# Kernel optimization log

Hardware: AMD Instinct MI355X
Metric: run time of the kernel (lower is better)

Reference implementation:

```python
import jax, jax.numpy as jnp
import numpy as np

B, S, E, H, D = 2, 2048, 768, 12, 64  # batch, seq, emb_dim, num_heads, encoder_emb_dim
EPS = 1e-5


def setup_inputs() -> dict:
    key = jax.random.key(0)
    ks = jax.random.split(key, 6)
    # kaiming-uniform-ish bound for fan_in=E
    bound = float(np.sqrt(6.0 / E))
    u = lambda k, shp: jax.random.uniform(k, shp, jnp.float32, -bound, bound)
    return {
        "x": jax.random.normal(ks[0], (B, S, E), jnp.float32),
        "ln_w": jnp.ones((E,), jnp.float32),
        "ln_b": jnp.zeros((E,), jnp.float32),
        "wq": u(ks[1], (E, H * D)),
        "bq": jnp.zeros((H * D,), jnp.float32),
        "wk": u(ks[2], (E, H * D)),
        "bk": jnp.zeros((H * D,), jnp.float32),
        "wv": u(ks[3], (E, H * D)),
        "bv": jnp.zeros((H * D,), jnp.float32),
        "wo": u(ks[4], (H * D, E)),
        "bo": jnp.zeros((E,), jnp.float32),
    }


def reference(x, ln_w, ln_b, wq, bq, wk, bk, wv, bv, wo, bo):
    b, s, _ = x.shape
    # LayerNorm (biased variance, eps=1e-5), as torch.nn.LayerNorm
    mu = x.mean(-1, keepdims=True)
    var = ((x - mu) ** 2).mean(-1, keepdims=True)
    xn = (x - mu) * jax.lax.rsqrt(var + EPS) * ln_w + ln_b

    q = (xn @ wq + bq).reshape(b, s, H, D)
    k = (xn @ wk + bk).reshape(b, s, H, D)
    v = (xn @ wv + bv).reshape(b, s, H, D)

    scale = 1.0 / np.sqrt(D).astype(np.float32)
    scores = jnp.einsum("bihd,bjhd->bhij", q, k) * scale  # [B,H,S,S]

    # masking=True, self_attending=True: mask STRICTLY lower triangle with -inf
    # (i.e. each position attends only to itself and FUTURE positions)
    mask = jnp.tril(jnp.ones((s, s), dtype=bool), k=-1)
    scores = jnp.where(mask, -jnp.inf, scores)

    a = jax.nn.softmax(scores, axis=-1)
    h = jnp.einsum("bhij,bjhd->bihd", a, v).reshape(b, s, H * D)
    return h @ wo + bo
```

## Files before the change

kernel.cpp:

```cpp
#include <hip/hip_runtime.h>

typedef __bf16 bf16_t;
typedef __bf16 bf16x8 __attribute__((ext_vector_type(8)));
typedef __bf16 bf16x4 __attribute__((ext_vector_type(4)));
typedef short  s16x4  __attribute__((ext_vector_type(4)));
typedef float  f32x4  __attribute__((ext_vector_type(4)));
typedef unsigned int u32;

#define BB 2
#define SS 2048
#define EE 768
#define HH 12
#define DD 64
#define NROW (BB*SS)

#define GLDS16(gp, lp) __builtin_amdgcn_global_load_lds( \
    (const __attribute__((address_space(1))) u32*)(gp),   \
    (__attribute__((address_space(3))) u32*)(lp), 16, 0, 0)

#if __has_builtin(__builtin_amdgcn_mfma_f32_16x16x16bf16_1k)
#define MFMA16_BUILTIN 1
static __device__ __forceinline__ f32x4 mfma_16x16x16_bf16(bf16x4 a, bf16x4 b, f32x4 c) {
  return __builtin_amdgcn_mfma_f32_16x16x16bf16_1k(
      __builtin_bit_cast(s16x4, a), __builtin_bit_cast(s16x4, b), c, 0, 0, 0);
}
#else
#define MFMA16_BUILTIN 0
static __device__ __forceinline__ f32x4 mfma_16x16x16_bf16(bf16x4 a, bf16x4 b, f32x4 c) {
  asm volatile("v_mfma_f32_16x16x16_bf16 %0, %1, %2, %0" : "+v"(c) : "v"(a), "v"(b));
  return c;
}
#endif

__global__ __launch_bounds__(256) void pack_w_kernel(
    const float* __restrict__ wq, const float* __restrict__ wk,
    const float* __restrict__ wv, const float* __restrict__ wo,
    bf16_t* __restrict__ wt)
{
  __shared__ float tile[64][65];
  const float* src = (blockIdx.z==0)?wq:(blockIdx.z==1)?wk:(blockIdx.z==2)?wv:wo;
  const int k0 = blockIdx.x*64, n0 = blockIdx.y*64;
  const int t = threadIdx.x;
  #pragma unroll
  for (int it=0; it<16; ++it) {
    int idx = it*256+t, r = idx>>6, c = idx&63;
    tile[r][c] = src[(size_t)(k0+r)*EE + n0 + c];
  }
  __syncthreads();
  bf16_t* dst = wt + (size_t)blockIdx.z*EE*EE;
  #pragma unroll
  for (int it=0; it<16; ++it) {
    int idx = it*256+t, r = idx>>6, c = idx&63;
    dst[(size_t)(n0+r)*EE + k0 + c] = (bf16_t)tile[c][r];
  }
}

__global__ __launch_bounds__(256) void ln_kernel(
    const float* __restrict__ x, const float* __restrict__ w,
    const float* __restrict__ bvec, bf16_t* __restrict__ xn)
{
  const int row = blockIdx.x, t = threadIdx.x;
  const float* xr = x + (size_t)row*EE;
  float v0 = xr[t], v1 = xr[t+256], v2 = xr[t+512];
  float s  = v0+v1+v2;
  float ss = v0*v0 + v1*v1 + v2*v2;
  #pragma unroll
  for (int m=1; m<64; m<<=1) { s += __shfl_xor(s,m); ss += __shfl_xor(ss,m); }
  __shared__ float red[2][4];
  const int wid = t>>6, lane = t&63;
  if (lane==0) { red[0][wid]=s; red[1][wid]=ss; }
  __syncthreads();
  s  = red[0][0]+red[0][1]+red[0][2]+red[0][3];
  ss = red[1][0]+red[1][1]+red[1][2]+red[1][3];
  const float mu   = s*(1.0f/EE);
  const float rstd = rsqrtf(ss*(1.0f/EE) - mu*mu + 1e-5f);
  bf16_t* xo = xn + (size_t)row*EE;
  xo[t      ] = (bf16_t)((v0-mu)*rstd*w[t      ] + bvec[t      ]);
  xo[t + 256] = (bf16_t)((v1-mu)*rstd*w[t + 256] + bvec[t + 256]);
  xo[t + 512] = (bf16_t)((v2-mu)*rstd*w[t + 512] + bvec[t + 512]);
}

__global__ __launch_bounds__(256) void gemm_qkv_kernel(
    const bf16_t* __restrict__ xn, const bf16_t* __restrict__ wt,
    const float* __restrict__ bq, const float* __restrict__ bk, const float* __restrict__ bv,
    bf16_t* __restrict__ qb, bf16_t* __restrict__ kb, bf16_t* __restrict__ vb)
{
  __shared__ __align__(16) bf16_t As[2][128][32];
  __shared__ __align__(16) bf16_t Bs[2][128][32];
  const int bm = blockIdx.x, by = blockIdx.y;
  const int mat = by/6, nb = by%6;
  const bf16_t* W = wt + (size_t)mat*EE*EE + (size_t)nb*128*EE;
  const float* bias = (mat==0)?bq:(mat==1)?bk:bv;
  bf16_t* outp = (mat==0)?qb:(mat==1)?kb:vb;
  const int t = threadIdx.x, lane = t&63, wid = t>>6;
  const int wr = wid>>1, wc = wid&1;
  const int lrow = lane&15, lk = lane>>4;
  const bf16_t* Ag = xn + (size_t)bm*128*EE;

  const int srow = t>>2, sp = t&3;
  const int sg = sp ^ ((srow>>1)&3);
  const int pcs = (lrow>>1)&3;

  auto stage = [&](int buf, int k0) {
    const bf16_t* asrc = Ag + (size_t)srow*EE + k0 + sg*8;
    const bf16_t* bsrc = W  + (size_t)srow*EE + k0 + sg*8;
    GLDS16(asrc,                 &As[buf][0][0] + t*8);
    GLDS16(asrc + (size_t)64*EE, &As[buf][0][0] + 2048 + t*8);
    GLDS16(bsrc,                 &Bs[buf][0][0] + t*8);
    GLDS16(bsrc + (size_t)64*EE, &Bs[buf][0][0] + 2048 + t*8);
  };

  f32x4 acc[4][4];
  #pragma unroll
  for (int i=0;i<4;++i)
    #pragma unroll
    for (int j=0;j<4;++j) acc[i][j] = (f32x4){0.f,0.f,0.f,0.f};

  stage(0, 0);
  __syncthreads();
  int cur = 0;
  for (int k0=0; k0<EE; k0+=32) {
    if (k0+32 < EE) stage(cur^1, k0+32);
    bf16x8 af[4], bfv[4];
    #pragma unroll
    for (int mi=0;mi<4;++mi) af[mi]  = *(const bf16x8*)&As[cur][wr*64+mi*16+lrow][(lk^pcs)*8];
    #pragma unroll
    for (int ni=0;ni<4;++ni) bfv[ni] = *(const bf16x8*)&Bs[cur][wc*64+ni*16+lrow][(lk^pcs)*8];
    #pragma unroll
    for (int mi=0;mi<4;++mi)
      #pragma unroll
      for (int ni=0;ni<4;++ni)
        acc[mi][ni] = __builtin_amdgcn_mfma_f32_16x16x32_bf16(af[mi], bfv[ni], acc[mi][ni], 0,0,0);
    __syncthreads();
    cur ^= 1;
  }
  const int m_base = bm*128 + wr*64;
  const int n_base = nb*128 + wc*64;
  #pragma unroll
  for (int ni=0;ni<4;++ni) {
    const int col = n_base + ni*16 + lrow;
    const float bias_v = bias[col];
    #pragma unroll
    for (int mi=0;mi<4;++mi) {
      #pragma unroll
      for (int r=0;r<4;++r) {
        int row = m_base + mi*16 + 4*lk + r;
        outp[(size_t)row*EE + col] = (bf16_t)(acc[mi][ni][r] + bias_v);
      }
    }
  }
}

__global__ __launch_bounds__(256) void vtrans_kernel(
    const bf16_t* __restrict__ v, bf16_t* __restrict__ vt)
{
  __shared__ __align__(16) bf16_t tile[64][72];
  const int j0 = blockIdx.x*64, bh = blockIdx.y;
  const int b = bh/HH, h = bh%HH;
  const int t = threadIdx.x;
  #pragma unroll
  for (int it=0; it<2; ++it) {
    int idx = it*256+t, r = idx>>3, c8 = (idx&7)*8;
    *(bf16x8*)&tile[r][c8] = *(const bf16x8*)(v + (size_t)(b*SS + j0 + r)*EE + h*DD + c8);
  }
  __syncthreads();
  #pragma unroll
  for (int it=0; it<2; ++it) {
    int idx = it*256+t, d = idx>>3, c8 = (idx&7)*8;
    bf16x8 val;
    #pragma unroll
    for (int i=0;i<8;++i) val[i] = tile[c8+i][d];
    *(bf16x8*)(vt + ((size_t)bh*DD + d)*SS + j0 + c8) = val;
  }
}

__global__ __launch_bounds__(256) void attn_kernel(
    const bf16_t* __restrict__ qb, const bf16_t* __restrict__ kb,
    const bf16_t* __restrict__ vt, bf16_t* __restrict__ hb)
{
  __shared__ __align__(16) bf16_t Ks[2][64][64];
  __shared__ __align__(16) bf16_t Vts[2][64][64];

  const int bid = blockIdx.x;
  const int rnd = bid >> 8, g = bid & 255;
  const int item = (rnd == 1) ? (511 - g) : (rnd*256 + g);
  const int qt = item / 24, bh = item % 24;

  const int i0 = qt*64, b = bh/HH, h = bh%HH;
  const int t = threadIdx.x, lane = t&63, wid = t>>6;
  const int lrow = lane&15, lk = lane>>4;

  const int srow = t>>3, sp = t&7;
  const int sgc = sp ^ (srow&7);
  const bf16_t* kbase  = kb + (size_t)b*SS*EE + h*DD;
  const bf16_t* vtbase = vt + (size_t)bh*DD*SS;

  const bf16_t* qrow = qb + (size_t)(b*SS + i0 + wid*16 + lrow)*EE + h*DD;
  const bf16x8 qf0 = *(const bf16x8*)(qrow + lk*8);
  const bf16x8 qf1 = *(const bf16x8*)(qrow + 32 + lk*8);

  f32x4 acc_ot[4];
  #pragma unroll
  for (int i=0;i<4;++i) acc_ot[i] = (f32x4){0.f,0.f,0.f,0.f};
  float lsum = 0.f;
  const int iloc = wid*16 + lrow;
  const int kkey = lrow&7;

  auto stage = [&](int buf, int jt) {
    const int j0v = jt*64;
    const bf16_t* ksrc = kbase  + (size_t)(j0v + srow)*EE + sgc*8;
    const bf16_t* vsrc = vtbase + (size_t)srow*SS + j0v + sgc*8;
    GLDS16(ksrc,                 &Ks[buf][0][0]  + t*8);
    GLDS16(ksrc + (size_t)32*EE, &Ks[buf][0][0]  + 2048 + t*8);
    GLDS16(vsrc,                 &Vts[buf][0][0] + t*8);
    GLDS16(vsrc + (size_t)32*SS, &Vts[buf][0][0] + 2048 + t*8);
  };

#define ATTN_TILE(CUR, MASKED) do {                                          \
    float e[4][4];                                                           \
    _Pragma("unroll")                                                        \
    for (int sj=0;sj<4;++sj) {                                               \
      const bf16_t* krow = &Ks[CUR][sj*16+lrow][0];                          \
      bf16x8 kf0 = *(const bf16x8*)(krow + ((lk^kkey)<<3));                  \
      bf16x8 kf1 = *(const bf16x8*)(krow + (((lk+4)^kkey)<<3));              \
      f32x4 a = (f32x4){0.f,0.f,0.f,0.f};                                    \
      a = __builtin_amdgcn_mfma_f32_16x16x32_bf16(kf0, qf0, a, 0,0,0);       \
      a = __builtin_amdgcn_mfma_f32_16x16x32_bf16(kf1, qf1, a, 0,0,0);       \
      _Pragma("unroll")                                                      \
      for (int r=0;r<4;++r) {                                                \
        float ee = a[r]*0.180336878f - 34.6246784f;                          \
        if (MASKED && (sj*16 + 4*lk + r) < iloc) ee = -1e30f;                \
        e[sj][r] = ee;                                                       \
      }                                                                      \
    }                                                                        \
    bf16x4 pb[4];                                                            \
    _Pragma("unroll")                                                        \
    for (int sj=0;sj<4;++sj)                                                 \
      _Pragma("unroll")                                                      \
      for (int r=0;r<4;++r) {                                                \
        float p = exp2f(e[sj][r]);                                           \
        lsum += p;                                                           \
        pb[sj][r] = (bf16_t)p;                                               \
      }                                                                      \
    _Pragma("unroll")                                                        \
    for (int sd=0;sd<4;++sd) {                                               \
      const bf16_t* vrow = &Vts[CUR][sd*16+lrow][0];                         \
      _Pragma("unroll")                                                      \
      for (int sj=0;sj<4;++sj) {                                             \
        bf16x4 vf = *(const bf16x4*)(vrow + (((2*sj+(lk>>1))^kkey)<<3) + ((lk&1)<<2)); \
        acc_ot[sd] = mfma_16x16x16_bf16(vf, pb[sj], acc_ot[sd]);             \
      }                                                                      \
    }                                                                        \
  } while(0)

  const int ntiles = SS/64 - qt;
  stage(0, qt);
  __syncthreads();
  if (ntiles > 1) stage(1, qt+1);
  ATTN_TILE(0, true);
#if !MFMA16_BUILTIN
  asm volatile("s_nop 7\n\ts_nop 7");
#endif
  __syncthreads();

  int cur = 1;
  for (int it2=1; it2<ntiles; ++it2) {
    if (it2+1 < ntiles) stage(cur^1, qt+it2+1);
    ATTN_TILE(cur, false);
#if !MFMA16_BUILTIN
    asm volatile("s_nop 7\n\ts_nop 7");
#endif
    __syncthreads();
    cur ^= 1;
  }
#undef ATTN_TILE

  lsum += __shfl_xor(lsum, 16);
  lsum += __shfl_xor(lsum, 32);
  const float inv = 1.0f / lsum;

  const int erow = wid*16 + lrow, ekey = erow&7;
  #pragma unroll
  for (int sd=0;sd<4;++sd) {
    bf16x4 ov;
    #pragma unroll
    for (int r=0;r<4;++r) ov[r] = (bf16_t)(acc_ot[sd][r] * inv);
    *(bf16x4*)(&Ks[0][erow][0] + (((2*sd+(lk>>1))^ekey)<<3) + ((lk&1)<<2)) = ov;
  }
  __syncthreads();
  const int rq = wid*16 + (lane>>2), rkey = rq&7, c4 = lane&3;
  bf16x8 o0 = *(const bf16x8*)(&Ks[0][rq][0] + (((2*c4  )^rkey)<<3));
  bf16x8 o1 = *(const bf16x8*)(&Ks[0][rq][0] + (((2*c4+1)^rkey)<<3));
  bf16_t* orow = hb + (size_t)(b*SS + i0 + rq)*EE + h*DD + c4*16;
  *(bf16x8*)orow = o0;
  *(bf16x8*)(orow+8) = o1;
}

__global__ __launch_bounds__(256) void gemm_out_kernel(
    const bf16_t* __restrict__ hbuf, const bf16_t* __restrict__ wto,
    const float* __restrict__ bo, float* __restrict__ out)
{
  __shared__ __align__(16) bf16_t As[2][128][32];
  __shared__ __align__(16) bf16_t Bs[2][128][32];
  const int bm = blockIdx.x, nb = blockIdx.y;
  const bf16_t* W = wto + (size_t)nb*128*EE;
  const int t = threadIdx.x, lane = t&63, wid = t>>6;
  const int wr = wid>>1, wc = wid&1;
  const int lrow = lane&15, lk = lane>>4;
  const bf16_t* Ag = hbuf + (size_t)bm*128*EE;

  const int srow = t>>2, sp = t&3;
  const int sg = sp ^ ((srow>>1)&3);
  const int pcs = (lrow>>1)&3;

  auto stage = [&](int buf, int k0) {
    const bf16_t* asrc = Ag + (size_t)srow*EE + k0 + sg*8;
    const bf16_t* bsrc = W  + (size_t)srow*EE + k0 + sg*8;
    GLDS16(asrc,                 &As[buf][0][0] + t*8);
    GLDS16(asrc + (size_t)64*EE, &As[buf][0][0] + 2048 + t*8);
    GLDS16(bsrc,                 &Bs[buf][0][0] + t*8);
    GLDS16(bsrc + (size_t)64*EE, &Bs[buf][0][0] + 2048 + t*8);
  };

  f32x4 acc[4][4];
  #pragma unroll
  for (int i=0;i<4;++i)
    #pragma unroll
    for (int j=0;j<4;++j) acc[i][j] = (f32x4){0.f,0.f,0.f,0.f};

  stage(0, 0);
  __syncthreads();
  int cur = 0;
  for (int k0=0; k0<EE; k0+=32) {
    if (k0+32 < EE) stage(cur^1, k0+32);
    bf16x8 af[4], bfv[4];
    #pragma unroll
    for (int mi=0;mi<4;++mi) af[mi]  = *(const bf16x8*)&As[cur][wr*64+mi*16+lrow][(lk^pcs)*8];
    #pragma unroll
    for (int ni=0;ni<4;++ni) bfv[ni] = *(const bf16x8*)&Bs[cur][wc*64+ni*16+lrow][(lk^pcs)*8];
    #pragma unroll
    for (int mi=0;mi<4;++mi)
      #pragma unroll
      for (int ni=0;ni<4;++ni)
        acc[mi][ni] = __builtin_amdgcn_mfma_f32_16x16x32_bf16(af[mi], bfv[ni], acc[mi][ni], 0,0,0);
    __syncthreads();
    cur ^= 1;
  }
  const int m_base = bm*128 + wr*64;
  const int n_base = nb*128 + wc*64;
  #pragma unroll
  for (int ni=0;ni<4;++ni) {
    const int col = n_base + ni*16 + lrow;
    const float bias_v = bo[col];
    #pragma unroll
    for (int mi=0;mi<4;++mi) {
      #pragma unroll
      for (int r=0;r<4;++r) {
        int row = m_base + mi*16 + 4*lk + r;
        out[(size_t)row*EE + col] = acc[mi][ni][r] + bias_v;
      }
    }
  }
}

extern "C" void kernel_launch(void* const* d_in, const int* in_sizes, int n_in,
                              void* d_out, int out_size, void* d_ws, size_t ws_size,
                              hipStream_t stream) {
  const float* x    = (const float*)d_in[0];
  const float* ln_w = (const float*)d_in[1];
  const float* ln_b = (const float*)d_in[2];
  const float* wq   = (const float*)d_in[3];
  const float* bq   = (const float*)d_in[4];
  const float* wk   = (const float*)d_in[5];
  const float* bk   = (const float*)d_in[6];
  const float* wv   = (const float*)d_in[7];
  const float* bv   = (const float*)d_in[8];
  const float* wo   = (const float*)d_in[9];
  const float* bo   = (const float*)d_in[10];
  float* out = (float*)d_out;

  char* ws = (char*)d_ws;
  bf16_t* wt  = (bf16_t*)(ws);
  bf16_t* xn  = (bf16_t*)(ws + 4718592);
  bf16_t* qb  = (bf16_t*)(ws + 11010048);
  bf16_t* kb  = (bf16_t*)(ws + 17301504);
  bf16_t* vb  = (bf16_t*)(ws + 23592960);
  bf16_t* vtb = (bf16_t*)(ws + 29884416);
  bf16_t* hb  = (bf16_t*)(ws + 36175872);

  pack_w_kernel  <<<dim3(12,12,4), 256, 0, stream>>>(wq, wk, wv, wo, wt);
  ln_kernel      <<<dim3(NROW),    256, 0, stream>>>(x, ln_w, ln_b, xn);
  gemm_qkv_kernel<<<dim3(32,18),   256, 0, stream>>>(xn, wt, bq, bk, bv, qb, kb, vb);
  vtrans_kernel  <<<dim3(32,24),   256, 0, stream>>>(vb, vtb);
  attn_kernel    <<<dim3(768),     256, 0, stream>>>(qb, kb, vtb, hb);
  gemm_out_kernel<<<dim3(32,6),    256, 0, stream>>>(hb, wt + (size_t)3*EE*EE, bo, out);
}
```

Before: 95.58 us.

## Use 2 waves per attention block with 32 query rows per wave

Halves the attention block to 128 threads, and each wave now handles two 16-row query groups. Every K and V fragment read from shared memory is reused for two MFMA chains, which halves LDS traffic per output and adds independent MFMA work per wave. Exp and masking are folded into the score loop, and the output goes through a dedicated padded LDS tile. The cost is more registers per thread and fewer waves per block to hide latency.

```diff
diff --git a/kernel.cpp b/kernel.cpp
--- a/kernel.cpp
+++ b/kernel.cpp
@@ -174,81 +174,87 @@
   }
 }
 
-__global__ __launch_bounds__(256) void attn_kernel(
+__global__ __launch_bounds__(128) void attn_kernel(
     const bf16_t* __restrict__ qb, const bf16_t* __restrict__ kb,
     const bf16_t* __restrict__ vt, bf16_t* __restrict__ hb)
 {
   __shared__ __align__(16) bf16_t Ks[2][64][64];
   __shared__ __align__(16) bf16_t Vts[2][64][64];
+  __shared__ __align__(16) bf16_t Os[64][72];
 
   const int bid = blockIdx.x;
-  const int rnd = bid >> 8, g = bid & 255;
-  const int item = (rnd == 1) ? (511 - g) : (rnd*256 + g);
+  const int rnd = bid >> 8, g8 = bid & 255;
+  const int item = (rnd == 1) ? (511 - g8) : (rnd*256 + g8);
   const int qt = item / 24, bh = item % 24;
 
   const int i0 = qt*64, b = bh/HH, h = bh%HH;
-  const int t = threadIdx.x, lane = t&63, wid = t>>6;
+  const int t = threadIdx.x, lane = t&63, w = t>>6;
   const int lrow = lane&15, lk = lane>>4;
 
-  const int srow = t>>3, sp = t&7;
-  const int sgc = sp ^ (srow&7);
+  const int sr = t>>3, sp = t&7;
+  const int sgc = sp ^ (sr&7);
   const bf16_t* kbase  = kb + (size_t)b*SS*EE + h*DD;
   const bf16_t* vtbase = vt + (size_t)bh*DD*SS;
 
-  const bf16_t* qrow = qb + (size_t)(b*SS + i0 + wid*16 + lrow)*EE + h*DD;
-  const bf16x8 qf0 = *(const bf16x8*)(qrow + lk*8);
-  const bf16x8 qf1 = *(const bf16x8*)(qrow + 32 + lk*8);
-
-  f32x4 acc_ot[4];
-  #pragma unroll
-  for (int i=0;i<4;++i) acc_ot[i] = (f32x4){0.f,0.f,0.f,0.f};
-  float lsum = 0.f;
-  const int iloc = wid*16 + lrow;
+  bf16x8 qf[2][2];
+  #pragma unroll
+  for (int g=0; g<2; ++g) {
+    const bf16_t* qrow = qb + (size_t)(b*SS + i0 + w*32 + g*16 + lrow)*EE + h*DD;
+    qf[g][0] = *(const bf16x8*)(qrow + lk*8);
+    qf[g][1] = *(const bf16x8*)(qrow + 32 + lk*8);
+  }
+
+  f32x4 acc[2][4];
+  #pragma unroll
+  for (int g=0; g<2; ++g)
+    #pragma unroll
+    for (int i=0;i<4;++i) acc[g][i] = (f32x4){0.f,0.f,0.f,0.f};
+  float lsum[2] = {0.f, 0.f};
   const int kkey = lrow&7;
 
   auto stage = [&](int buf, int jt) {
     const int j0v = jt*64;
-    const bf16_t* ksrc = kbase  + (size_t)(j0v + srow)*EE + sgc*8;
-    const bf16_t* vsrc = vtbase + (size_t)srow*SS + j0v + sgc*8;
-    GLDS16(ksrc,                 &Ks[buf][0][0]  + t*8);
-    GLDS16(ksrc + (size_t)32*EE, &Ks[buf][0][0]  + 2048 + t*8);
-    GLDS16(vsrc,                 &Vts[buf][0][0] + t*8);
-    GLDS16(vsrc + (size_t)32*SS, &Vts[buf][0][0] + 2048 + t*8);
+    #pragma unroll
+    for (int i=0;i<4;++i)
+      GLDS16(kbase + (size_t)(j0v + i*16 + sr)*EE + sgc*8,
+             &Ks[buf][0][0] + (i*128 + t)*8);
+    #pragma unroll
+    for (int i=0;i<4;++i)
+      GLDS16(vtbase + (size_t)(i*16 + sr)*SS + j0v + sgc*8,
+             &Vts[buf][0][0] + (i*128 + t)*8);
   };
 
 #define ATTN_TILE(CUR, MASKED) do {                                          \
-    float e[4][4];                                                           \
+    bf16x4 pb[2][4];                                                         \
     _Pragma("unroll")                                                        \
     for (int sj=0;sj<4;++sj) {                                               \
       const bf16_t* krow = &Ks[CUR][sj*16+lrow][0];                          \
       bf16x8 kf0 = *(const bf16x8*)(krow + ((lk^kkey)<<3));                  \
       bf16x8 kf1 = *(const bf16x8*)(krow + (((lk+4)^kkey)<<3));              \
-      f32x4 a = (f32x4){0.f,0.f,0.f,0.f};                                    \
-      a = __builtin_amdgcn_mfma_f32_16x16x32_bf16(kf0, qf0, a, 0,0,0);       \
-      a = __builtin_amdgcn_mfma_f32_16x16x32_bf16(kf1, qf1, a, 0,0,0);       \
       _Pragma("unroll")                                                      \
-      for (int r=0;r<4;++r) {                                                \
-        float ee = a[r]*0.180336878f - 34.6246784f;                          \
-        if (MASKED && (sj*16 + 4*lk + r) < iloc) ee = -1e30f;                \
-        e[sj][r] = ee;                                                       \
+      for (int g=0; g<2; ++g) {                                              \
+        f32x4 a = (f32x4){0.f,0.f,0.f,0.f};                                  \
+        a = __builtin_amdgcn_mfma_f32_16x16x32_bf16(kf0, qf[g][0], a, 0,0,0);\
+        a = __builtin_amdgcn_mfma_f32_16x16x32_bf16(kf1, qf[g][1], a, 0,0,0);\
+        const int iloc = w*32 + g*16 + lrow;                                 \
+        _Pragma("unroll")                                                    \
+        for (int r=0;r<4;++r) {                                              \
+          float ee = a[r]*0.180336878f - 34.6246784f;                        \
+          if (MASKED && (sj*16 + 4*lk + r) < iloc) ee = -1e30f;              \
+          float p = exp2f(ee);                                               \
+          lsum[g] += p;                                                      \
+          pb[g][sj][r] = (bf16_t)p;                                          \
+        }                                                                    \
       }                                                                      \
     }                                                                        \
-    bf16x4 pb[4];                                                            \
-    _Pragma("unroll")                                                        \
-    for (int sj=0;sj<4;++sj)                                                 \
-      _Pragma("unroll")                                                      \
-      for (int r=0;r<4;++r) {                                                \
-        float p = exp2f(e[sj][r]);                                           \
-        lsum += p;                                                           \
-        pb[sj][r] = (bf16_t)p;                                               \
-      }                                                                      \
     _Pragma("unroll")                                                        \
     for (int sd=0;sd<4;++sd) {                                               \
       const bf16_t* vrow = &Vts[CUR][sd*16+lrow][0];                         \
       _Pragma("unroll")                                                      \
       for (int sj=0;sj<4;++sj) {                                             \
         bf16x4 vf = *(const bf16x4*)(vrow + (((2*sj+(lk>>1))^kkey)<<3) + ((lk&1)<<2)); \
-        acc_ot[sd] = mfma_16x16x16_bf16(vf, pb[sj], acc_ot[sd]);             \
+        acc[0][sd] = mfma_16x16x16_bf16(vf, pb[0][sj], acc[0][sd]);          \
+        acc[1][sd] = mfma_16x16x16_bf16(vf, pb[1][sj], acc[1][sd]);          \
       }                                                                      \
     }                                                                        \
   } while(0)
@@ -275,25 +281,30 @@
   }
 #undef ATTN_TILE
 
-  lsum += __shfl_xor(lsum, 16);
-  lsum += __shfl_xor(lsum, 32);
-  const float inv = 1.0f / lsum;
-
-  const int erow = wid*16 + lrow, ekey = erow&7;
-  #pragma unroll
-  for (int sd=0;sd<4;++sd) {
-    bf16x4 ov;
-    #pragma unroll
-    for (int r=0;r<4;++r) ov[r] = (bf16_t)(acc_ot[sd][r] * inv);
-    *(bf16x4*)(&Ks[0][erow][0] + (((2*sd+(lk>>1))^ekey)<<3) + ((lk&1)<<2)) = ov;
-  }
-  __syncthreads();
-  const int rq = wid*16 + (lane>>2), rkey = rq&7, c4 = lane&3;
-  bf16x8 o0 = *(const bf16x8*)(&Ks[0][rq][0] + (((2*c4  )^rkey)<<3));
-  bf16x8 o1 = *(const bf16x8*)(&Ks[0][rq][0] + (((2*c4+1)^rkey)<<3));
-  bf16_t* orow = hb + (size_t)(b*SS + i0 + rq)*EE + h*DD + c4*16;
-  *(bf16x8*)orow = o0;
-  *(bf16x8*)(orow+8) = o1;
+  #pragma unroll
+  for (int g=0; g<2; ++g) {
+    lsum[g] += __shfl_xor(lsum[g], 16);
+    lsum[g] += __shfl_xor(lsum[g], 32);
+  }
+
+  #pragma unroll
+  for (int g=0; g<2; ++g) {
+    const float inv = 1.0f / lsum[g];
+    const int erow = w*32 + g*16 + lrow;
+    #pragma unroll
+    for (int sd=0;sd<4;++sd) {
+      bf16x4 ov;
+      #pragma unroll
+      for (int r=0;r<4;++r) ov[r] = (bf16_t)(acc[g][sd][r] * inv);
+      *(bf16x4*)&Os[erow][sd*16 + 4*lk] = ov;
+    }
+  }
+  __syncthreads();
+  const int rq = t>>1, half = t&1;
+  bf16_t* orow = hb + (size_t)(b*SS + i0 + rq)*EE + h*DD + half*32;
+  #pragma unroll
+  for (int k=0;k<4;++k)
+    *(bf16x8*)(orow + k*8) = *(const bf16x8*)&Os[rq][half*32 + k*8];
 }
 
 __global__ __launch_bounds__(256) void gemm_out_kernel(
@@ -392,6 +403,6 @@
   ln_kernel      <<<dim3(NROW),    256, 0, stream>>>(x, ln_w, ln_b, xn);
   gemm_qkv_kernel<<<dim3(32,18),   256, 0, stream>>>(xn, wt, bq, bk, bv, qb, kb, vb);
   vtrans_kernel  <<<dim3(32,24),   256, 0, stream>>>(vb, vtb);
-  attn_kernel    <<<dim3(768),     256, 0, stream>>>(qb, kb, vtb, hb);
+  attn_kernel    <<<dim3(768),     128, 0, stream>>>(qb, kb, vtb, hb);
   gemm_out_kernel<<<dim3(32,6),    256, 0, stream>>>(hb, wt + (size_t)3*EE*EE, bo, out);
 }
```

Result: slower. 106.9 us (+11.8%).
